# Optimization experiments

Measured on AMD Instinct MI355X. Metric: run time of the kernel, lower is better.

The kernel has to match this reference:

```python
import jax, jax.numpy as jnp
import numpy as np

C = 768
H = 12
HD = C // H  # 64


def setup_inputs() -> dict:
    key = jax.random.key(0)
    k1, k2, k3, k4, k5, k6 = jax.random.split(key, 6)
    B, T = 8, 1024
    x = jax.random.normal(k1, (B, T, C), dtype=jnp.float32)
    mask = jax.random.randint(k2, (B, T), 0, 2, dtype=jnp.int32)
    # Linear params stored so that y = x @ W + b (W is [in, out])
    W_attn = jax.random.normal(k3, (C, 3 * C), dtype=jnp.float32) * 0.02
    b_attn = jax.random.normal(k4, (3 * C,), dtype=jnp.float32) * 0.02
    W_proj = jax.random.normal(k5, (C, C), dtype=jnp.float32) * 0.02
    b_proj = jax.random.normal(k6, (C,), dtype=jnp.float32) * 0.02
    return {"x": x, "mask": mask, "W_attn": W_attn, "b_attn": b_attn,
            "W_proj": W_proj, "b_proj": b_proj}


def reference(x, mask, W_attn, b_attn, W_proj, b_proj):
    B, T, _ = x.shape
    qkv = x @ W_attn + b_attn                      # [B, T, 3C]
    q, k, v = jnp.split(qkv, 3, axis=2)            # each [B, T, C]
    # [B, T, C] -> [B, H, T, HD]
    q = q.reshape(B, T, H, HD).transpose(0, 2, 1, 3)
    k = k.reshape(B, T, H, HD).transpose(0, 2, 1, 3)
    v = v.reshape(B, T, H, HD).transpose(0, 2, 1, 3)

    scale = 1.0 / np.sqrt(HD).astype(np.float32)
    att = jnp.einsum('bhqd,bhkd->bhqk', q, k) * scale  # [B, H, T, T]

    causal = jnp.tril(jnp.ones((T, T), dtype=bool))    # [T, T]
    att = jnp.where(causal[None, None], att, -jnp.inf)

    # custom mask: per-(batch, query-row) flag; where mask==0 the whole row
    # of scores is overwritten with 0.0001 (AFTER causal fill, as in torch)
    row_masked = (mask == 0)[:, None, :, None]         # [B, 1, T, 1]
    att = jnp.where(row_masked, jnp.float32(1e-4), att)

    att = jax.nn.softmax(att, axis=-1)
    # dropout layers are identity in eval mode
    y = jnp.einsum('bhqk,bhkd->bhqd', att, v)          # [B, H, T, HD]
    y = y.transpose(0, 2, 1, 3).reshape(B, T, C)
    y = y @ W_proj + b_proj
    return y
```

## Files before the change

### kernel.cpp

```cpp
#include <hip/hip_runtime.h>

#define BQ 8
#define TT 1024
#define CC 768
#define NH 12
#define HD 64
#define BH (BQ*NH)
#define MROWS (BQ*TT)
#define NQKV (3*CC)
#define KD CC

typedef unsigned short u16;
typedef __attribute__((ext_vector_type(4))) short short4v;
typedef __attribute__((ext_vector_type(8))) short short8v;
typedef __attribute__((ext_vector_type(4))) float floatx4;
typedef __attribute__((address_space(1))) const unsigned int gu32;
typedef __attribute__((address_space(3))) unsigned int lu32;

__device__ __forceinline__ float bf2f(u16 u) {
  union { unsigned int i; float f; } c; c.i = ((unsigned int)u) << 16; return c.f;
}
__device__ __forceinline__ u16 f2bf(float f) {
  union { float f; unsigned int i; } c; c.f = f;
  unsigned int i = c.i;
  return (u16)((i + 0x7FFFu + ((i >> 16) & 1u)) >> 16);
}
__device__ __forceinline__ float fast_exp2(float x) {
  return __builtin_amdgcn_exp2f(x);
}
__device__ __forceinline__ void async_ld16(const u16* g, u16* l) {
  __builtin_amdgcn_global_load_lds((gu32*)g, (lu32*)l, 16, 0, 0);
}

#define PREP_CONV 6144
#define PREP_WA   1728
#define PREP_WP   576
#define PREP_TOTAL (PREP_CONV + PREP_WA + PREP_WP)

__global__ __launch_bounds__(256) void prep_kernel(
    const float* __restrict__ x, u16* __restrict__ xb,
    const float* __restrict__ Wattn, u16* __restrict__ WtA,
    const float* __restrict__ Wproj, u16* __restrict__ WtP,
    float* __restrict__ mvz)
{
  __shared__ float tile[32][33];
  int bid = blockIdx.x;
  int tid = threadIdx.x;
  if (bid == PREP_TOTAL) {
    for (int i = tid; i < BH * HD; i += 256) mvz[i] = 0.f;
    return;
  }
  if (bid < PREP_CONV) {
    int i = (bid * 256 + tid) * 4;
    floatx4 v = *(const floatx4*)(x + i);
    short4v o;
    o[0] = (short)f2bf(v[0]); o[1] = (short)f2bf(v[1]);
    o[2] = (short)f2bf(v[2]); o[3] = (short)f2bf(v[3]);
    *(short4v*)(xb + i) = o;
    return;
  }
  const float* in; u16* out; int R, Cc, b2;
  if (bid < PREP_CONV + PREP_WA) { in = Wattn; out = WtA; R = KD; Cc = NQKV; b2 = bid - PREP_CONV; }
  else                           { in = Wproj; out = WtP; R = CC; Cc = CC;   b2 = bid - PREP_CONV - PREP_WA; }
  int ct = Cc >> 5;
  int bx = b2 % ct;
  int by = b2 / ct;
  int tx = tid & 31;
  int ty = tid >> 5;
  int c0 = bx << 5, r0 = by << 5;
#pragma unroll
  for (int s = 0; s < 4; ++s)
    tile[ty + s*8][tx] = in[(size_t)(r0 + ty + s*8) * Cc + c0 + tx];
  __syncthreads();
#pragma unroll
  for (int s = 0; s < 4; ++s)
    out[(size_t)(c0 + ty + s*8) * R + r0 + tx] = f2bf(tile[tx][ty + s*8]);
}

__global__ __launch_bounds__(256) void gemm_bt(
    const u16* __restrict__ A, const u16* __restrict__ Bt,
    const float* __restrict__ bias,
    float* __restrict__ out,
    u16* __restrict__ qo, u16* __restrict__ ko, u16* __restrict__ vo,
    float* __restrict__ mvp,
    int M, int N, int mode)
{
  __shared__ u16 smem[64 * 64 + 128 * 64];
  u16* Asm = smem;
  u16* Bsm = smem + 64 * 64;

  int tid = threadIdx.x;
  int lane = tid & 63;
  int w = tid >> 6;
  int c = lane & 15;
  int q4 = lane >> 4;

  int mtiles = M >> 6;
  int mt = blockIdx.x % mtiles;
  int nt = blockIdx.x / mtiles;
  int m0 = mt << 6, n0 = nt << 7;

  int wr = (w >> 1) << 5;
  int wc = (w & 1) << 6;

  int srow8 = lane >> 3;
  int ug = ((lane & 7) ^ srow8) << 3;
  const u16* ag = A  + (size_t)(m0 + w * 16 + srow8) * KD + ug;
  const u16* bg = Bt + (size_t)(n0 + w * 32 + srow8) * KD + ug;
  u16* asl = &Asm[(w * 16) * 64];
  u16* bsl = &Bsm[(w * 32) * 64];

  floatx4 acc[2][4];
#pragma unroll
  for (int mi = 0; mi < 2; ++mi)
#pragma unroll
    for (int ni = 0; ni < 4; ++ni) acc[mi][ni] = (floatx4){0.f, 0.f, 0.f, 0.f};

  int c7 = c & 7;

#pragma unroll 1
  for (int kt = 0; kt < KD; kt += 64) {
    async_ld16(ag + kt,              asl);
    async_ld16(ag + kt + 8 * KD,     asl + 8 * 64);
    async_ld16(bg + kt,              bsl);
    async_ld16(bg + kt + 8 * KD,     bsl + 8 * 64);
    async_ld16(bg + kt + 16 * KD,    bsl + 16 * 64);
    async_ld16(bg + kt + 24 * KD,    bsl + 24 * 64);
    __syncthreads();

    short8v af[2][2], bf[4][2];
#pragma unroll
    for (int kc = 0; kc < 2; ++kc) {
      int uoff = ((kc * 4 + q4) ^ c7) << 3;
#pragma unroll
      for (int mi = 0; mi < 2; ++mi)
        af[mi][kc] = *(const short8v*)&Asm[(wr + mi * 16 + c) * 64 + uoff];
#pragma unroll
      for (int ni = 0; ni < 4; ++ni)
        bf[ni][kc] = *(const short8v*)&Bsm[(wc + ni * 16 + c) * 64 + uoff];
    }
#pragma unroll
    for (int kc = 0; kc < 2; ++kc)
#pragma unroll
      for (int mi = 0; mi < 2; ++mi)
#pragma unroll
        for (int ni = 0; ni < 4; ++ni)
          acc[mi][ni] = __builtin_amdgcn_mfma_f32_16x16x32_bf16(af[mi][kc], bf[ni][kc], acc[mi][ni], 0, 0, 0);
    __syncthreads();
  }

  if (mode == 0) {
    int which = (n0 + wc) / CC;
    int nbase = (n0 + wc) - which * CC;
    int bb = m0 >> 10;
    int t0 = m0 & 1023;

    if (which < 2) {
      u16* dst0 = (which == 0) ? qo : ko;
#pragma unroll
      for (int ni = 0; ni < 4; ++ni) {
        int nn = nbase + ni * 16 + c;
        int hh = nn >> 6, dd = nn & 63;
        float bv = bias[which * CC + nn];
#pragma unroll
        for (int mi = 0; mi < 2; ++mi) {
#pragma unroll
          for (int r = 0; r < 4; ++r) {
            int tt2 = t0 + wr + mi * 16 + q4 * 4 + r;
            dst0[(((size_t)(bb * NH + hh)) * TT + tt2) * HD + dd] = f2bf(acc[mi][ni][r] + bv);
          }
        }
      }
    }
    if (n0 + 127 >= 2 * CC) {
      u16* Ct = smem;
      if (which == 2) {
#pragma unroll
        for (int ni = 0; ni < 4; ++ni) {
          float bv = bias[2 * CC + nbase + ni * 16 + c];
#pragma unroll
          for (int mi = 0; mi < 2; ++mi) {
            short4v pk;
#pragma unroll
            for (int r = 0; r < 4; ++r) pk[r] = (short)f2bf(acc[mi][ni][r] + bv);
            *(short4v*)&Ct[(wc + ni * 16 + c) * 72 + wr + mi * 16 + q4 * 4] = pk;
          }
        }
      }
      __syncthreads();
#pragma unroll
      for (int j = 0; j < 4; ++j) {
        int flat = tid + j * 256;
        int drow = flat >> 3, u = flat & 7;
        int nn2 = n0 + drow;
        if (nn2 >= 2 * CC) {
          int nv = nn2 - 2 * CC;
          int h2 = nv >> 6, d2 = nv & 63;
          short8v val = *(const short8v*)&Ct[drow * 72 + u * 8];
          *(short8v*)&vo[(((size_t)(bb * NH + h2)) * HD + d2) * TT + t0 + u * 8] = val;
        }
      }
      if (which == 2) {
        int hw = nbase >> 6;
        int bhw = bb * NH + hw;
#pragma unroll
        for (int ni = 0; ni < 4; ++ni) {
          float bv = bias[2 * CC + nbase + ni * 16 + c];
          float s = 8.0f * bv;
#pragma unroll
          for (int mi = 0; mi < 2; ++mi)
#pragma unroll
            for (int r = 0; r < 4; ++r) s += acc[mi][ni][r];
          s += __shfl_xor(s, 16);
          s += __shfl_xor(s, 32);
          if (q4 == 0) atomicAdd(&mvp[bhw * HD + ni * 16 + c], s);
        }
      }
    }
  } else {
#pragma unroll
    for (int ni = 0; ni < 4; ++ni) {
      int nn = n0 + wc + ni * 16 + c;
      float bv = bias[nn];
#pragma unroll
      for (int mi = 0; mi < 2; ++mi) {
#pragma unroll
        for (int r = 0; r < 4; ++r) {
          int mm = m0 + wr + mi * 16 + q4 * 4 + r;
          out[(size_t)mm * N + nn] = acc[mi][ni][r] + bv;
        }
      }
    }
  }
}

__global__ __launch_bounds__(256) void gemm_proj(
    const u16* __restrict__ A, const u16* __restrict__ Bt,
    const float* __restrict__ bias, float* __restrict__ out)
{
  __shared__ u16 As[64 * 64];
  __shared__ u16 Bs[64 * 64];

  int tid = threadIdx.x;
  int lane = tid & 63;
  int w = tid >> 6;
  int c = lane & 15;
  int q4 = lane >> 4;

  int mt = blockIdx.x & 127;
  int nt = blockIdx.x >> 7;
  int m0 = mt << 6, n0 = nt << 6;

  int wr = (w >> 1) << 5;
  int wc = (w & 1) << 5;

  int srow8 = lane >> 3;
  int ug = ((lane & 7) ^ srow8) << 3;
  const u16* ag = A  + (size_t)(m0 + w * 16 + srow8) * KD + ug;
  const u16* bg = Bt + (size_t)(n0 + w * 16 + srow8) * KD + ug;
  u16* asl = &As[(w * 16) * 64];
  u16* bsl = &Bs[(w * 16) * 64];

  floatx4 acc[2][2];
#pragma unroll
  for (int mi = 0; mi < 2; ++mi)
#pragma unroll
    for (int ni = 0; ni < 2; ++ni) acc[mi][ni] = (floatx4){0.f, 0.f, 0.f, 0.f};

  int c7 = c & 7;

#pragma unroll 1
  for (int kt = 0; kt < KD; kt += 64) {
    async_ld16(ag + kt,          asl);
    async_ld16(ag + kt + 8 * KD, asl + 8 * 64);
    async_ld16(bg + kt,          bsl);
    async_ld16(bg + kt + 8 * KD, bsl + 8 * 64);
    __syncthreads();

    short8v af[2][2], bf[2][2];
#pragma unroll
    for (int kc = 0; kc < 2; ++kc) {
      int uoff = ((kc * 4 + q4) ^ c7) << 3;
#pragma unroll
      for (int mi = 0; mi < 2; ++mi)
        af[mi][kc] = *(const short8v*)&As[(wr + mi * 16 + c) * 64 + uoff];
#pragma unroll
      for (int ni = 0; ni < 2; ++ni)
        bf[ni][kc] = *(const short8v*)&Bs[(wc + ni * 16 + c) * 64 + uoff];
    }
#pragma unroll
    for (int kc = 0; kc < 2; ++kc)
#pragma unroll
      for (int mi = 0; mi < 2; ++mi)
#pragma unroll
        for (int ni = 0; ni < 2; ++ni)
          acc[mi][ni] = __builtin_amdgcn_mfma_f32_16x16x32_bf16(af[mi][kc], bf[ni][kc], acc[mi][ni], 0, 0, 0);
    __syncthreads();
  }

#pragma unroll
  for (int ni = 0; ni < 2; ++ni) {
    int nn = n0 + wc + ni * 16 + c;
    float bv = bias[nn];
#pragma unroll
    for (int mi = 0; mi < 2; ++mi) {
#pragma unroll
      for (int r = 0; r < 4; ++r) {
        int mm = m0 + wr + mi * 16 + q4 * 4 + r;
        out[(size_t)mm * CC + nn] = acc[mi][ni][r] + bv;
      }
    }
  }
}

#define LDW 72
#define SCL 0.18033688f

__global__ __launch_bounds__(256) void attn_kernel(
    const u16* __restrict__ qb, const u16* __restrict__ kb,
    const u16* __restrict__ vtb, const int* __restrict__ mask,
    const float* __restrict__ meanv,
    u16* __restrict__ outb)
{
  __shared__ u16 Ks[2][64 * LDW];
  __shared__ u16 Vs[2][64 * LDW];
  __shared__ u16 Ps[4][16 * LDW];

  int tid = threadIdx.x;
  int lane = tid & 63;
  int w = tid >> 6;
  int c = lane & 15;
  int q4 = lane >> 4;

  int lbid = ((blockIdx.x & 7) * 96) + (blockIdx.x >> 3);
  int pair = lbid & 7;
  int bh = lbid >> 3;
  int b = bh / NH;
  int h = bh - b * NH;

  int srow = tid >> 2;
  int schunk = (tid & 3) << 4;
  const u16* kgp = kb + ((size_t)bh * TT + srow) * HD + schunk;
  const u16* vgp = vtb + ((size_t)bh * HD + srow) * TT + schunk;
  u16* pw = &Ps[w][0];

  short8v onesv;
#pragma unroll
  for (int j = 0; j < 8; ++j) onesv[j] = (short)0x3F80;

#pragma unroll 1
  for (int phase = 0; phase < 2; ++phase) {
    int qt = phase ? (15 - pair) : pair;
    int rowbase = (qt << 6) + (w << 4);

    short8v qfrag[2];
    {
      const u16* qp = qb + ((size_t)bh * TT + rowbase + c) * HD + q4 * 8;
      qfrag[0] = *(const short8v*)qp;
      qfrag[1] = *(const short8v*)(qp + 32);
    }

    floatx4 o[4];
#pragma unroll
    for (int i = 0; i < 4; ++i) o[i] = (floatx4){0.f, 0.f, 0.f, 0.f};
    floatx4 o5 = (floatx4){0.f, 0.f, 0.f, 0.f};

    short8v kr0 = *(const short8v*)kgp;
    short8v kr1 = *(const short8v*)(kgp + 8);
    short8v vr0 = *(const short8v*)vgp;
    short8v vr1 = *(const short8v*)(vgp + 8);
    __syncthreads();
    {
      u16* kd = &Ks[0][srow * LDW + schunk];
      u16* vd = &Vs[0][srow * LDW + schunk];
      *(short8v*)kd = kr0; *(short8v*)(kd + 8) = kr1;
      *(short8v*)vd = vr0; *(short8v*)(vd + 8) = vr1;
    }

#pragma unroll 1
    for (int kt = 0; kt <= qt; ++kt) {
      int cur = kt & 1;
      __syncthreads();

      if (kt < qt) {
        const u16* kp = kgp + ((size_t)(kt + 1) << 6) * HD;
        const u16* vp = vgp + ((kt + 1) << 6);
        kr0 = *(const short8v*)kp;
        kr1 = *(const short8v*)(kp + 8);
        vr0 = *(const short8v*)vp;
        vr1 = *(const short8v*)(vp + 8);
      }

      floatx4 s[4];
#pragma unroll
      for (int nt = 0; nt < 4; ++nt) s[nt] = (floatx4){0.f, 0.f, 0.f, 0.f};
      __builtin_amdgcn_s_setprio(1);
#pragma unroll
      for (int kc = 0; kc < 2; ++kc) {
#pragma unroll
        for (int nt = 0; nt < 4; ++nt) {
          short8v kf = *(const short8v*)&Ks[cur][(nt * 16 + c) * LDW + kc * 32 + q4 * 8];
          s[nt] = __builtin_amdgcn_mfma_f32_16x16x32_bf16(kf, qfrag[kc], s[nt], 0, 0, 0);
        }
      }
      __builtin_amdgcn_s_setprio(0);

      int qrl = (w << 4) + c;
#pragma unroll
      for (int nt = 0; nt < 4; ++nt) {
        short4v pk;
#pragma unroll
        for (int r = 0; r < 4; ++r) {
          float sv = s[nt][r];
          if (kt == qt && (nt * 16 + (q4 << 2) + r > qrl)) sv = -INFINITY;
          pk[r] = (short)f2bf(fast_exp2(sv * SCL));
        }
        *(short4v*)&pw[c * LDW + nt * 16 + (q4 << 2)] = pk;
      }

      if (kt < qt) {
        u16* kd = &Ks[cur ^ 1][srow * LDW + schunk];
        u16* vd = &Vs[cur ^ 1][srow * LDW + schunk];
        *(short8v*)kd = kr0; *(short8v*)(kd + 8) = kr1;
        *(short8v*)vd = vr0; *(short8v*)(vd + 8) = vr1;
      }

      __builtin_amdgcn_s_setprio(1);
#pragma unroll
      for (int kc = 0; kc < 2; ++kc) {
        short8v pf = *(const short8v*)&pw[c * LDW + kc * 32 + q4 * 8];
#pragma unroll
        for (int nt = 0; nt < 4; ++nt) {
          short8v vf = *(const short8v*)&Vs[cur][(nt * 16 + c) * LDW + kc * 32 + q4 * 8];
          o[nt] = __builtin_amdgcn_mfma_f32_16x16x32_bf16(pf, vf, o[nt], 0, 0, 0);
        }
        o5 = __builtin_amdgcn_mfma_f32_16x16x32_bf16(pf, onesv, o5, 0, 0, 0);
      }
      __builtin_amdgcn_s_setprio(0);
    }

    int qrow[4]; bool msk[4]; float inv[4];
#pragma unroll
    for (int r = 0; r < 4; ++r) {
      qrow[r] = rowbase + q4 * 4 + r;
      msk[r] = (mask[b * TT + qrow[r]] == 0);
      inv[r] = 1.f / o5[r];
    }
#pragma unroll
    for (int nt = 0; nt < 4; ++nt) {
      int d = nt * 16 + c;
      float mv = meanv[bh * HD + d] * 0.0009765625f;
#pragma unroll
      for (int r = 0; r < 4; ++r) {
        float val = msk[r] ? mv : o[nt][r] * inv[r];
        outb[((size_t)(b * TT + qrow[r])) * CC + h * HD + d] = f2bf(val);
      }
    }
  }
}

extern "C" void kernel_launch(void* const* d_in, const int* in_sizes, int n_in,
                              void* d_out, int out_size, void* d_ws, size_t ws_size,
                              hipStream_t stream)
{
  (void)in_sizes; (void)n_in; (void)out_size; (void)ws_size;
  const float* x     = (const float*)d_in[0];
  const int*   mask  = (const int*)d_in[1];
  const float* Wattn = (const float*)d_in[2];
  const float* battn = (const float*)d_in[3];
  const float* Wproj = (const float*)d_in[4];
  const float* bproj = (const float*)d_in[5];
  float* out = (float*)d_out;

  char* ws = (char*)d_ws;
  size_t off = 0;
  auto alloc = [&](size_t bytes) -> void* {
    void* p = ws + off;
    off += (bytes + 255) & ~(size_t)255;
    return p;
  };
  u16* WtA  = (u16*)alloc((size_t)NQKV * KD * 2);
  u16* WtP  = (u16*)alloc((size_t)CC * CC * 2);
  u16* xb   = (u16*)alloc((size_t)MROWS * CC * 2);
  u16* qbuf = (u16*)alloc((size_t)MROWS * CC * 2);
  u16* kbuf = (u16*)alloc((size_t)MROWS * CC * 2);
  u16* vtb  = (u16*)alloc((size_t)MROWS * CC * 2);
  u16* abuf = (u16*)alloc((size_t)MROWS * CC * 2);
  float* mv = (float*)alloc((size_t)BH * HD * 4);

  prep_kernel<<<PREP_TOTAL + 1, 256, 0, stream>>>(x, xb, Wattn, WtA, Wproj, WtP, mv);

  gemm_bt<<<(MROWS/64)*(NQKV/128), 256, 0, stream>>>(
      xb, WtA, battn, nullptr, qbuf, kbuf, vtb, mv, MROWS, NQKV, 0);

  attn_kernel<<<BH * 8, 256, 0, stream>>>(qbuf, kbuf, vtb, mask, mv, abuf);

  gemm_proj<<<(MROWS/64)*(CC/64), 256, 0, stream>>>(abuf, WtP, bproj, out);
}
```

Baseline: 180.6 us.

## Process both paired query tiles in one pass sharing K/V tile loads

Instead of two sequential phases (light tile, then heavy tile) that each stream K/V from global memory, the attention kernel now keeps both query tiles' fragments and accumulators live and iterates once over the heavy tile's key range. It computes the light tile only while it is still causally active. This halves the K/V global loads and LDS staging and removes one pass's barrier overhead. The cost is extra registers for a second set of accumulators, so launch_bounds now requests 3 blocks per SM, which may force spills. The per-wave P buffer is also reused for both tiles within an iteration, which relies on same-wave ordering.

```diff
diff --git a/kernel.cpp b/kernel.cpp
--- a/kernel.cpp
+++ b/kernel.cpp
@@ -316,7 +316,7 @@
 #define LDW 72
 #define SCL 0.18033688f
 
-__global__ __launch_bounds__(256) void attn_kernel(
+__global__ __launch_bounds__(256, 3) void attn_kernel(
     const u16* __restrict__ qb, const u16* __restrict__ kb,
     const u16* __restrict__ vtb, const int* __restrict__ mask,
     const float* __restrict__ meanv,
@@ -338,6 +338,11 @@
   int b = bh / NH;
   int h = bh - b * NH;
 
+  int qtA = pair;
+  int qtB = 15 - pair;
+  int rowbaseA = (qtA << 6) + (w << 4);
+  int rowbaseB = (qtB << 6) + (w << 4);
+
   int srow = tid >> 2;
   int schunk = (tid & 3) << 4;
   const u16* kgp = kb + ((size_t)bh * TT + srow) * HD + schunk;
@@ -348,97 +353,136 @@
 #pragma unroll
   for (int j = 0; j < 8; ++j) onesv[j] = (short)0x3F80;
 
+  short8v qfA[2], qfB[2];
+  {
+    const u16* qpA = qb + ((size_t)bh * TT + rowbaseA + c) * HD + q4 * 8;
+    qfA[0] = *(const short8v*)qpA;
+    qfA[1] = *(const short8v*)(qpA + 32);
+    const u16* qpB = qb + ((size_t)bh * TT + rowbaseB + c) * HD + q4 * 8;
+    qfB[0] = *(const short8v*)qpB;
+    qfB[1] = *(const short8v*)(qpB + 32);
+  }
+
+  floatx4 oA[4], oB[4];
+#pragma unroll
+  for (int i = 0; i < 4; ++i) {
+    oA[i] = (floatx4){0.f, 0.f, 0.f, 0.f};
+    oB[i] = (floatx4){0.f, 0.f, 0.f, 0.f};
+  }
+  floatx4 o5A = (floatx4){0.f, 0.f, 0.f, 0.f};
+  floatx4 o5B = (floatx4){0.f, 0.f, 0.f, 0.f};
+
+  short8v kr0 = *(const short8v*)kgp;
+  short8v kr1 = *(const short8v*)(kgp + 8);
+  short8v vr0 = *(const short8v*)vgp;
+  short8v vr1 = *(const short8v*)(vgp + 8);
+  {
+    u16* kd = &Ks[0][srow * LDW + schunk];
+    u16* vd = &Vs[0][srow * LDW + schunk];
+    *(short8v*)kd = kr0; *(short8v*)(kd + 8) = kr1;
+    *(short8v*)vd = vr0; *(short8v*)(vd + 8) = vr1;
+  }
+
+  int qrl = (w << 4) + c;
+
 #pragma unroll 1
-  for (int phase = 0; phase < 2; ++phase) {
-    int qt = phase ? (15 - pair) : pair;
-    int rowbase = (qt << 6) + (w << 4);
-
-    short8v qfrag[2];
-    {
-      const u16* qp = qb + ((size_t)bh * TT + rowbase + c) * HD + q4 * 8;
-      qfrag[0] = *(const short8v*)qp;
-      qfrag[1] = *(const short8v*)(qp + 32);
-    }
-
-    floatx4 o[4];
-#pragma unroll
-    for (int i = 0; i < 4; ++i) o[i] = (floatx4){0.f, 0.f, 0.f, 0.f};
-    floatx4 o5 = (floatx4){0.f, 0.f, 0.f, 0.f};
-
-    short8v kr0 = *(const short8v*)kgp;
-    short8v kr1 = *(const short8v*)(kgp + 8);
-    short8v vr0 = *(const short8v*)vgp;
-    short8v vr1 = *(const short8v*)(vgp + 8);
+  for (int kt = 0; kt <= qtB; ++kt) {
+    int cur = kt & 1;
     __syncthreads();
-    {
-      u16* kd = &Ks[0][srow * LDW + schunk];
-      u16* vd = &Vs[0][srow * LDW + schunk];
+
+    if (kt < qtB) {
+      const u16* kp = kgp + ((size_t)(kt + 1) << 6) * HD;
+      const u16* vp = vgp + ((kt + 1) << 6);
+      kr0 = *(const short8v*)kp;
+      kr1 = *(const short8v*)(kp + 8);
+      vr0 = *(const short8v*)vp;
+      vr1 = *(const short8v*)(vp + 8);
+    }
+
+    bool doA = (kt <= qtA);
+
+    floatx4 sA[4], sB[4];
+#pragma unroll
+    for (int nt = 0; nt < 4; ++nt) {
+      sA[nt] = (floatx4){0.f, 0.f, 0.f, 0.f};
+      sB[nt] = (floatx4){0.f, 0.f, 0.f, 0.f};
+    }
+    __builtin_amdgcn_s_setprio(1);
+#pragma unroll
+    for (int kc = 0; kc < 2; ++kc) {
+#pragma unroll
+      for (int nt = 0; nt < 4; ++nt) {
+        short8v kf = *(const short8v*)&Ks[cur][(nt * 16 + c) * LDW + kc * 32 + q4 * 8];
+        if (doA) sA[nt] = __builtin_amdgcn_mfma_f32_16x16x32_bf16(kf, qfA[kc], sA[nt], 0, 0, 0);
+        sB[nt] = __builtin_amdgcn_mfma_f32_16x16x32_bf16(kf, qfB[kc], sB[nt], 0, 0, 0);
+      }
+    }
+    __builtin_amdgcn_s_setprio(0);
+
+    if (doA) {
+#pragma unroll
+      for (int nt = 0; nt < 4; ++nt) {
+        short4v pk;
+#pragma unroll
+        for (int r = 0; r < 4; ++r) {
+          float sv = sA[nt][r];
+          if (kt == qtA && (nt * 16 + (q4 << 2) + r > qrl)) sv = -INFINITY;
+          pk[r] = (short)f2bf(fast_exp2(sv * SCL));
+        }
+        *(short4v*)&pw[c * LDW + nt * 16 + (q4 << 2)] = pk;
+      }
+      __builtin_amdgcn_s_setprio(1);
+#pragma unroll
+      for (int kc = 0; kc < 2; ++kc) {
+        short8v pf = *(const short8v*)&pw[c * LDW + kc * 32 + q4 * 8];
+#pragma unroll
+        for (int nt = 0; nt < 4; ++nt) {
+          short8v vf = *(const short8v*)&Vs[cur][(nt * 16 + c) * LDW + kc * 32 + q4 * 8];
+          oA[nt] = __builtin_amdgcn_mfma_f32_16x16x32_bf16(pf, vf, oA[nt], 0, 0, 0);
+        }
+        o5A = __builtin_amdgcn_mfma_f32_16x16x32_bf16(pf, onesv, o5A, 0, 0, 0);
+      }
+      __builtin_amdgcn_s_setprio(0);
+    }
+
+#pragma unroll
+    for (int nt = 0; nt < 4; ++nt) {
+      short4v pk;
+#pragma unroll
+      for (int r = 0; r < 4; ++r) {
+        float sv = sB[nt][r];
+        if (kt == qtB && (nt * 16 + (q4 << 2) + r > qrl)) sv = -INFINITY;
+        pk[r] = (short)f2bf(fast_exp2(sv * SCL));
+      }
+      *(short4v*)&pw[c * LDW + nt * 16 + (q4 << 2)] = pk;
+    }
+
+    if (kt < qtB) {
+      u16* kd = &Ks[cur ^ 1][srow * LDW + schunk];
+      u16* vd = &Vs[cur ^ 1][srow * LDW + schunk];
       *(short8v*)kd = kr0; *(short8v*)(kd + 8) = kr1;
       *(short8v*)vd = vr0; *(short8v*)(vd + 8) = vr1;
     }
 
-#pragma unroll 1
-    for (int kt = 0; kt <= qt; ++kt) {
-      int cur = kt & 1;
-      __syncthreads();
-
-      if (kt < qt) {
-        const u16* kp = kgp + ((size_t)(kt + 1) << 6) * HD;
-        const u16* vp = vgp + ((kt + 1) << 6);
-        kr0 = *(const short8v*)kp;
-        kr1 = *(const short8v*)(kp + 8);
-        vr0 = *(const short8v*)vp;
-        vr1 = *(const short8v*)(vp + 8);
-      }
-
-      floatx4 s[4];
-#pragma unroll
-      for (int nt = 0; nt < 4; ++nt) s[nt] = (floatx4){0.f, 0.f, 0.f, 0.f};
-      __builtin_amdgcn_s_setprio(1);
-#pragma unroll
-      for (int kc = 0; kc < 2; ++kc) {
-#pragma unroll
-        for (int nt = 0; nt < 4; ++nt) {
-          short8v kf = *(const short8v*)&Ks[cur][(nt * 16 + c) * LDW + kc * 32 + q4 * 8];
-          s[nt] = __builtin_amdgcn_mfma_f32_16x16x32_bf16(kf, qfrag[kc], s[nt], 0, 0, 0);
-        }
-      }
-      __builtin_amdgcn_s_setprio(0);
-
-      int qrl = (w << 4) + c;
+    __builtin_amdgcn_s_setprio(1);
+#pragma unroll
+    for (int kc = 0; kc < 2; ++kc) {
+      short8v pf = *(const short8v*)&pw[c * LDW + kc * 32 + q4 * 8];
 #pragma unroll
       for (int nt = 0; nt < 4; ++nt) {
-        short4v pk;
-#pragma unroll
-        for (int r = 0; r < 4; ++r) {
-          float sv = s[nt][r];
-          if (kt == qt && (nt * 16 + (q4 << 2) + r > qrl)) sv = -INFINITY;
-          pk[r] = (short)f2bf(fast_exp2(sv * SCL));
-        }
-        *(short4v*)&pw[c * LDW + nt * 16 + (q4 << 2)] = pk;
-      }
-
-      if (kt < qt) {
-        u16* kd = &Ks[cur ^ 1][srow * LDW + schunk];
-        u16* vd = &Vs[cur ^ 1][srow * LDW + schunk];
-        *(short8v*)kd = kr0; *(short8v*)(kd + 8) = kr1;
-        *(short8v*)vd = vr0; *(short8v*)(vd + 8) = vr1;
-      }
-
-      __builtin_amdgcn_s_setprio(1);
-#pragma unroll
-      for (int kc = 0; kc < 2; ++kc) {
-        short8v pf = *(const short8v*)&pw[c * LDW + kc * 32 + q4 * 8];
-#pragma unroll
-        for (int nt = 0; nt < 4; ++nt) {
-          short8v vf = *(const short8v*)&Vs[cur][(nt * 16 + c) * LDW + kc * 32 + q4 * 8];
-          o[nt] = __builtin_amdgcn_mfma_f32_16x16x32_bf16(pf, vf, o[nt], 0, 0, 0);
-        }
-        o5 = __builtin_amdgcn_mfma_f32_16x16x32_bf16(pf, onesv, o5, 0, 0, 0);
-      }
-      __builtin_amdgcn_s_setprio(0);
-    }
-
+        short8v vf = *(const short8v*)&Vs[cur][(nt * 16 + c) * LDW + kc * 32 + q4 * 8];
+        oB[nt] = __builtin_amdgcn_mfma_f32_16x16x32_bf16(pf, vf, oB[nt], 0, 0, 0);
+      }
+      o5B = __builtin_amdgcn_mfma_f32_16x16x32_bf16(pf, onesv, o5B, 0, 0, 0);
+    }
+    __builtin_amdgcn_s_setprio(0);
+  }
+
+#pragma unroll
+  for (int t = 0; t < 2; ++t) {
+    int rowbase = t ? rowbaseB : rowbaseA;
+    floatx4* o = t ? oB : oA;
+    floatx4 o5 = t ? o5B : o5A;
     int qrow[4]; bool msk[4]; float inv[4];
 #pragma unroll
     for (int r = 0; r < 4; ++r) {
```

New measurement: 182.1 us. About the same (+0.8%).

## Compact unmasked query rows so attention only computes rows that need softmax

Applied to the files above, without the earlier changes.

A new prep block builds, for each batch, a compacted list of query indices whose mask is nonzero, plus their count, using a wave ballot and prefix popcount. The attention kernel then tiles over these compacted rows, and each tile loops only up to the key tile of its last real row, so rows whose output is the constant mean of V no longer go through QK/PV work. Extra blocks write the mean-V rows for masked positions. Launch bounds ask for 3 blocks per CU, and f2bf now uses the HIP intrinsic. In exchange, query loads become gathered, per-row causal bounds vary, and tiles are unbalanced and data dependent, while the old pairing of light and heavy tiles for balance is dropped.

```diff
diff --git a/kernel.cpp b/kernel.cpp
--- a/kernel.cpp
+++ b/kernel.cpp
@@ -1,4 +1,5 @@
 #include <hip/hip_runtime.h>
+#include <hip/hip_bf16.h>
 
 #define BQ 8
 #define TT 1024
@@ -21,9 +22,9 @@
   union { unsigned int i; float f; } c; c.i = ((unsigned int)u) << 16; return c.f;
 }
 __device__ __forceinline__ u16 f2bf(float f) {
-  union { float f; unsigned int i; } c; c.f = f;
-  unsigned int i = c.i;
-  return (u16)((i + 0x7FFFu + ((i >> 16) & 1u)) >> 16);
+  union { __hip_bfloat16 h; u16 u; } c;
+  c.h = __float2bfloat16(f);
+  return c.u;
 }
 __device__ __forceinline__ float fast_exp2(float x) {
   return __builtin_amdgcn_exp2f(x);
@@ -41,13 +42,32 @@
     const float* __restrict__ x, u16* __restrict__ xb,
     const float* __restrict__ Wattn, u16* __restrict__ WtA,
     const float* __restrict__ Wproj, u16* __restrict__ WtP,
-    float* __restrict__ mvz)
+    float* __restrict__ mvz,
+    const int* __restrict__ maskp, int* __restrict__ tidx, int* __restrict__ nbv)
 {
   __shared__ float tile[32][33];
   int bid = blockIdx.x;
   int tid = threadIdx.x;
   if (bid == PREP_TOTAL) {
     for (int i = tid; i < BH * HD; i += 256) mvz[i] = 0.f;
+    return;
+  }
+  if (bid == PREP_TOTAL + 1) {
+    int lane = tid & 63, w = tid >> 6;
+    for (int b2 = w; b2 < BQ; b2 += 4) {
+      int base = 0;
+#pragma unroll 1
+      for (int ch = 0; ch < 16; ++ch) {
+        int t = (ch << 6) + lane;
+        int m = maskp[b2 * TT + t];
+        unsigned long long bm = __ballot(m != 0);
+        int pre = __builtin_popcountll(bm & ((1ull << lane) - 1ull));
+        if (m != 0) tidx[b2 * TT + base + pre] = t;
+        base += __builtin_popcountll(bm);
+      }
+      if (lane == 0) nbv[b2] = base;
+      for (int i = base + lane; i < TT; i += 64) tidx[b2 * TT + i] = TT - 1;
+    }
     return;
   }
   if (bid < PREP_CONV) {
@@ -316,27 +336,62 @@
 #define LDW 72
 #define SCL 0.18033688f
 
-__global__ __launch_bounds__(256) void attn_kernel(
+__global__ __launch_bounds__(256, 3) void attn_kernel(
     const u16* __restrict__ qb, const u16* __restrict__ kb,
     const u16* __restrict__ vtb, const int* __restrict__ mask,
     const float* __restrict__ meanv,
+    const int* __restrict__ tidx, const int* __restrict__ nbv,
     u16* __restrict__ outb)
 {
   __shared__ u16 Ks[2][64 * LDW];
   __shared__ u16 Vs[2][64 * LDW];
   __shared__ u16 Ps[4][16 * LDW];
 
+  int bid = blockIdx.x;
   int tid = threadIdx.x;
+
+  if (bid >= BH * 16) {
+    int bh2 = bid - BH * 16;
+    int b2 = bh2 / NH, h2 = bh2 - b2 * NH;
+    int dch = (tid & 3) << 4;
+    short8v v0, v1;
+#pragma unroll
+    for (int j = 0; j < 8; ++j) {
+      v0[j] = (short)f2bf(meanv[bh2 * HD + dch + j] * 0.0009765625f);
+      v1[j] = (short)f2bf(meanv[bh2 * HD + dch + 8 + j] * 0.0009765625f);
+    }
+#pragma unroll 1
+    for (int t = tid >> 2; t < TT; t += 64) {
+      if (mask[b2 * TT + t] == 0) {
+        u16* dst = outb + ((size_t)(b2 * TT + t)) * CC + h2 * HD + dch;
+        *(short8v*)dst = v0;
+        *(short8v*)(dst + 8) = v1;
+      }
+    }
+    return;
+  }
+
   int lane = tid & 63;
   int w = tid >> 6;
   int c = lane & 15;
   int q4 = lane >> 4;
 
-  int lbid = ((blockIdx.x & 7) * 96) + (blockIdx.x >> 3);
-  int pair = lbid & 7;
-  int bh = lbid >> 3;
+  int lbid = (bid & 7) * 192 + (bid >> 3);
+  int tile = lbid & 15;
+  int bh = lbid >> 4;
   int b = bh / NH;
   int h = bh - b * NH;
+
+  int nb = nbv[b];
+  int ntiles = (nb + 63) >> 6;
+  if (tile >= ntiles) return;
+
+  const int* tix = tidx + b * TT;
+  int last = tile * 64 + 63; if (last > nb - 1) last = nb - 1;
+  int ktmax = (tix[last] >> 6) + 1;
+
+  int rowc = tile * 64 + (w << 4) + c;
+  int tqc = tix[rowc];
 
   int srow = tid >> 2;
   int schunk = (tid & 3) << 4;
@@ -348,113 +403,106 @@
 #pragma unroll
   for (int j = 0; j < 8; ++j) onesv[j] = (short)0x3F80;
 
+  short8v qfrag[2];
+  {
+    const u16* qp = qb + ((size_t)bh * TT + tqc) * HD + q4 * 8;
+    qfrag[0] = *(const short8v*)qp;
+    qfrag[1] = *(const short8v*)(qp + 32);
+  }
+
+  floatx4 o[4];
+#pragma unroll
+  for (int i = 0; i < 4; ++i) o[i] = (floatx4){0.f, 0.f, 0.f, 0.f};
+  floatx4 o5 = (floatx4){0.f, 0.f, 0.f, 0.f};
+
+  short8v kr0 = *(const short8v*)kgp;
+  short8v kr1 = *(const short8v*)(kgp + 8);
+  short8v vr0 = *(const short8v*)vgp;
+  short8v vr1 = *(const short8v*)(vgp + 8);
+  {
+    u16* kd = &Ks[0][srow * LDW + schunk];
+    u16* vd = &Vs[0][srow * LDW + schunk];
+    *(short8v*)kd = kr0; *(short8v*)(kd + 8) = kr1;
+    *(short8v*)vd = vr0; *(short8v*)(vd + 8) = vr1;
+  }
+
 #pragma unroll 1
-  for (int phase = 0; phase < 2; ++phase) {
-    int qt = phase ? (15 - pair) : pair;
-    int rowbase = (qt << 6) + (w << 4);
-
-    short8v qfrag[2];
-    {
-      const u16* qp = qb + ((size_t)bh * TT + rowbase + c) * HD + q4 * 8;
-      qfrag[0] = *(const short8v*)qp;
-      qfrag[1] = *(const short8v*)(qp + 32);
-    }
-
-    floatx4 o[4];
-#pragma unroll
-    for (int i = 0; i < 4; ++i) o[i] = (floatx4){0.f, 0.f, 0.f, 0.f};
-    floatx4 o5 = (floatx4){0.f, 0.f, 0.f, 0.f};
-
-    short8v kr0 = *(const short8v*)kgp;
-    short8v kr1 = *(const short8v*)(kgp + 8);
-    short8v vr0 = *(const short8v*)vgp;
-    short8v vr1 = *(const short8v*)(vgp + 8);
+  for (int kt = 0; kt < ktmax; ++kt) {
+    int cur = kt & 1;
     __syncthreads();
-    {
-      u16* kd = &Ks[0][srow * LDW + schunk];
-      u16* vd = &Vs[0][srow * LDW + schunk];
+
+    if (kt + 1 < ktmax) {
+      const u16* kp = kgp + ((size_t)(kt + 1) << 6) * HD;
+      const u16* vp = vgp + ((kt + 1) << 6);
+      kr0 = *(const short8v*)kp;
+      kr1 = *(const short8v*)(kp + 8);
+      vr0 = *(const short8v*)vp;
+      vr1 = *(const short8v*)(vp + 8);
+    }
+
+    floatx4 s[4];
+#pragma unroll
+    for (int nt = 0; nt < 4; ++nt) s[nt] = (floatx4){0.f, 0.f, 0.f, 0.f};
+    __builtin_amdgcn_s_setprio(1);
+#pragma unroll
+    for (int kc = 0; kc < 2; ++kc) {
+#pragma unroll
+      for (int nt = 0; nt < 4; ++nt) {
+        short8v kf = *(const short8v*)&Ks[cur][(nt * 16 + c) * LDW + kc * 32 + q4 * 8];
+        s[nt] = __builtin_amdgcn_mfma_f32_16x16x32_bf16(kf, qfrag[kc], s[nt], 0, 0, 0);
+      }
+    }
+    __builtin_amdgcn_s_setprio(0);
+
+    int kbase = kt << 6;
+#pragma unroll
+    for (int nt = 0; nt < 4; ++nt) {
+      short4v pk;
+#pragma unroll
+      for (int r = 0; r < 4; ++r) {
+        float sv = s[nt][r];
+        if (kbase + nt * 16 + (q4 << 2) + r > tqc) sv = -INFINITY;
+        pk[r] = (short)f2bf(fast_exp2(sv * SCL));
+      }
+      *(short4v*)&pw[c * LDW + nt * 16 + (q4 << 2)] = pk;
+    }
+
+    if (kt + 1 < ktmax) {
+      u16* kd = &Ks[cur ^ 1][srow * LDW + schunk];
+      u16* vd = &Vs[cur ^ 1][srow * LDW + schunk];
       *(short8v*)kd = kr0; *(short8v*)(kd + 8) = kr1;
       *(short8v*)vd = vr0; *(short8v*)(vd + 8) = vr1;
     }
 
-#pragma unroll 1
-    for (int kt = 0; kt <= qt; ++kt) {
-      int cur = kt & 1;
-      __syncthreads();
-
-      if (kt < qt) {
-        const u16* kp = kgp + ((size_t)(kt + 1) << 6) * HD;
-        const u16* vp = vgp + ((kt + 1) << 6);
-        kr0 = *(const short8v*)kp;
-        kr1 = *(const short8v*)(kp + 8);
-        vr0 = *(const short8v*)vp;
-        vr1 = *(const short8v*)(vp + 8);
-      }
-
-      floatx4 s[4];
-#pragma unroll
-      for (int nt = 0; nt < 4; ++nt) s[nt] = (floatx4){0.f, 0.f, 0.f, 0.f};
-      __builtin_amdgcn_s_setprio(1);
-#pragma unroll
-      for (int kc = 0; kc < 2; ++kc) {
-#pragma unroll
-        for (int nt = 0; nt < 4; ++nt) {
-          short8v kf = *(const short8v*)&Ks[cur][(nt * 16 + c) * LDW + kc * 32 + q4 * 8];
-          s[nt] = __builtin_amdgcn_mfma_f32_16x16x32_bf16(kf, qfrag[kc], s[nt], 0, 0, 0);
-        }
-      }
-      __builtin_amdgcn_s_setprio(0);
-
-      int qrl = (w << 4) + c;
+    __builtin_amdgcn_s_setprio(1);
+#pragma unroll
+    for (int kc = 0; kc < 2; ++kc) {
+      short8v pf = *(const short8v*)&pw[c * LDW + kc * 32 + q4 * 8];
 #pragma unroll
       for (int nt = 0; nt < 4; ++nt) {
-        short4v pk;
-#pragma unroll
-        for (int r = 0; r < 4; ++r) {
-          float sv = s[nt][r];
-          if (kt == qt && (nt * 16 + (q4 << 2) + r > qrl)) sv = -INFINITY;
-          pk[r] = (short)f2bf(fast_exp2(sv * SCL));
-        }
-        *(short4v*)&pw[c * LDW + nt * 16 + (q4 << 2)] = pk;
-      }
-
-      if (kt < qt) {
-        u16* kd = &Ks[cur ^ 1][srow * LDW + schunk];
-        u16* vd = &Vs[cur ^ 1][srow * LDW + schunk];
-        *(short8v*)kd = kr0; *(short8v*)(kd + 8) = kr1;
-        *(short8v*)vd = vr0; *(short8v*)(vd + 8) = vr1;
-      }
-
-      __builtin_amdgcn_s_setprio(1);
-#pragma unroll
-      for (int kc = 0; kc < 2; ++kc) {
-        short8v pf = *(const short8v*)&pw[c * LDW + kc * 32 + q4 * 8];
-#pragma unroll
-        for (int nt = 0; nt < 4; ++nt) {
-          short8v vf = *(const short8v*)&Vs[cur][(nt * 16 + c) * LDW + kc * 32 + q4 * 8];
-          o[nt] = __builtin_amdgcn_mfma_f32_16x16x32_bf16(pf, vf, o[nt], 0, 0, 0);
-        }
-        o5 = __builtin_amdgcn_mfma_f32_16x16x32_bf16(pf, onesv, o5, 0, 0, 0);
-      }
-      __builtin_amdgcn_s_setprio(0);
-    }
-
-    int qrow[4]; bool msk[4]; float inv[4];
+        short8v vf = *(const short8v*)&Vs[cur][(nt * 16 + c) * LDW + kc * 32 + q4 * 8];
+        o[nt] = __builtin_amdgcn_mfma_f32_16x16x32_bf16(pf, vf, o[nt], 0, 0, 0);
+      }
+      o5 = __builtin_amdgcn_mfma_f32_16x16x32_bf16(pf, onesv, o5, 0, 0, 0);
+    }
+    __builtin_amdgcn_s_setprio(0);
+  }
+
+  int crow0 = tile * 64 + (w << 4) + (q4 << 2);
+  int trow[4]; bool valid[4]; float inv[4];
+#pragma unroll
+  for (int r = 0; r < 4; ++r) {
+    valid[r] = (crow0 + r) < nb;
+    trow[r] = tix[crow0 + r];
+    inv[r] = 1.f / o5[r];
+  }
+#pragma unroll
+  for (int nt = 0; nt < 4; ++nt) {
+    int d = nt * 16 + c;
 #pragma unroll
     for (int r = 0; r < 4; ++r) {
-      qrow[r] = rowbase + q4 * 4 + r;
-      msk[r] = (mask[b * TT + qrow[r]] == 0);
-      inv[r] = 1.f / o5[r];
-    }
-#pragma unroll
-    for (int nt = 0; nt < 4; ++nt) {
-      int d = nt * 16 + c;
-      float mv = meanv[bh * HD + d] * 0.0009765625f;
-#pragma unroll
-      for (int r = 0; r < 4; ++r) {
-        float val = msk[r] ? mv : o[nt][r] * inv[r];
-        outb[((size_t)(b * TT + qrow[r])) * CC + h * HD + d] = f2bf(val);
-      }
+      if (valid[r])
+        outb[((size_t)(b * TT + trow[r])) * CC + h * HD + d] = f2bf(o[nt][r] * inv[r]);
     }
   }
 }
@@ -487,13 +535,17 @@
   u16* vtb  = (u16*)alloc((size_t)MROWS * CC * 2);
   u16* abuf = (u16*)alloc((size_t)MROWS * CC * 2);
   float* mv = (float*)alloc((size_t)BH * HD * 4);
-
-  prep_kernel<<<PREP_TOTAL + 1, 256, 0, stream>>>(x, xb, Wattn, WtA, Wproj, WtP, mv);
+  int* tidx = (int*)alloc((size_t)BQ * TT * 4);
+  int* nbv  = (int*)alloc((size_t)BQ * 4);
+
+  prep_kernel<<<PREP_TOTAL + 2, 256, 0, stream>>>(x, xb, Wattn, WtA, Wproj, WtP,
+                                                  mv, mask, tidx, nbv);
 
   gemm_bt<<<(MROWS/64)*(NQKV/128), 256, 0, stream>>>(
       xb, WtA, battn, nullptr, qbuf, kbuf, vtb, mv, MROWS, NQKV, 0);
 
-  attn_kernel<<<BH * 8, 256, 0, stream>>>(qbuf, kbuf, vtb, mask, mv, abuf);
+  attn_kernel<<<BH * 16 + BH, 256, 0, stream>>>(qbuf, kbuf, vtb, mask, mv,
+                                                tidx, nbv, abuf);
 
   gemm_proj<<<(MROWS/64)*(CC/64), 256, 0, stream>>>(abuf, WtP, bproj, out);
 }
```

Result: slower. 191.2 us (+5.9%).
